# Kernel optimization log

Measured on AMD Instinct MI355X. Metric: run time of the kernel, lower is better.

The kernel has to match this reference:

```python
import jax, jax.numpy as jnp
import numpy as np


def setup_inputs() -> dict:
    key = jax.random.key(0)
    ks = jax.random.split(key, 7)
    B, L, D, H = 256, 1024, 768, 768
    x = jax.random.normal(ks[0], (B, L, D), dtype=jnp.float32)
    label_mask = jax.random.randint(ks[1], (B, L), 0, 2).astype(jnp.int32)
    global_prototype_tensor = jax.random.normal(ks[2], (L + 1, D), dtype=jnp.float32)
    W_h = jax.random.normal(ks[3], (H, D), dtype=jnp.float32) * 0.02
    b_h = jax.random.normal(ks[4], (H,), dtype=jnp.float32) * 0.02
    W_p = jax.random.normal(ks[5], (D, H), dtype=jnp.float32) * 0.02
    b_p = jax.random.normal(ks[6], (D,), dtype=jnp.float32) * 0.02
    return {"x": x, "label_mask": label_mask,
            "global_prototype_tensor": global_prototype_tensor,
            "W_h": W_h, "b_h": b_h, "W_p": W_p, "b_p": b_p}


def _mlp(v, W_h, b_h, W_p, b_p):
    # torch Linear: y = v @ W.T + b
    h = jax.nn.relu(jnp.einsum('ld,hd->lh', v, W_h) + b_h)
    return jnp.einsum('lh,dh->ld', h, W_p) + b_p


def reference(x, label_mask, global_prototype_tensor, W_h, b_h, W_p, b_p):
    # x: [B, L, D]; label_mask: [B, L] (1 if label i in example's label_list)
    m = label_mask.astype(x.dtype)                        # [B, L]
    pos_cnt = m.sum(0)                                    # [L]
    B = x.shape[0]
    anti_cnt = B - pos_cnt                                # [L]
    pos_sum = jnp.einsum('bl,bld->ld', m, x)              # masked segment-sum
    tot_sum = x.sum(0)                                    # [L, D]
    anti_sum = tot_sum - pos_sum

    pos_mean = pos_sum / jnp.maximum(pos_cnt, 1.0)[:, None]
    anti_mean = anti_sum / jnp.maximum(anti_cnt, 1.0)[:, None]

    avg_pos = 0.5 * pos_mean + 0.5 * global_prototype_tensor[:-1]   # [L, D]
    avg_anti = 0.5 * anti_mean + 0.5 * global_prototype_tensor[-1]  # [L, D]

    proto = _mlp(avg_pos, W_h, b_h, W_p, b_p)
    proto = jnp.where((pos_cnt > 0)[:, None], proto, 0.0)           # rows stay zero if no members

    anti_proto = _mlp(avg_anti, W_h, b_h, W_p, b_p)
    w = (anti_cnt > 0).astype(x.dtype)                              # [L]
    anti = jnp.einsum('l,ld->d', w, anti_proto) / jnp.maximum(w.sum(), 1.0)

    return jnp.concatenate([proto, anti[None, :]], axis=0)          # [L+1, D]
```

## Files before the change

### kernel.cpp

```cpp
#include <hip/hip_runtime.h>

#define L_DIM 1024
#define B_DIM 256
#define D_DIM 768
#define K_DIM 768
#define NT    (K_DIM / 32)

typedef short short8 __attribute__((ext_vector_type(8)));
typedef float floatx4 __attribute__((ext_vector_type(4)));

__device__ __forceinline__ ushort f2bf(float f) {
    union { float f; unsigned u; } v; v.f = f;
    unsigned r = v.u + 0x7FFF + ((v.u >> 16) & 1);
    return (ushort)(r >> 16);
}
__device__ __forceinline__ float bf2f(ushort h) {
    union { unsigned u; float f; } v; v.u = ((unsigned)h) << 16;
    return v.f;
}

__device__ __forceinline__ void gl16(const ushort* g, ushort* l) {
    __builtin_amdgcn_global_load_lds(
        (const __attribute__((address_space(1))) unsigned int*)g,
        (__attribute__((address_space(3))) unsigned int*)l, 16, 0, 0);
}

__global__ __launch_bounds__(768)
void reduce_build_v(const float* __restrict__ x,
                    const int* __restrict__ mask,
                    const float* __restrict__ gpt,
                    ushort* __restrict__ Vhi, ushort* __restrict__ Vlo,
                    float* __restrict__ pos_cnt)
{
    __shared__ int mS[256][4];

    const int l0  = blockIdx.x * 4;
    const int tid = threadIdx.x;

    if (tid < 256)
        *(int4*)&mS[tid][0] = *(const int4*)(mask + (size_t)tid * L_DIM + l0);
    __syncthreads();

    const int row = tid / 192;
    const int t   = tid % 192;
    const int d0  = t * 4;
    const int l   = l0 + row;

    const size_t bstride = (size_t)L_DIM * D_DIM;
    const float* xp = x + (size_t)l * D_DIM + d0;

    float4 pos = make_float4(0.f, 0.f, 0.f, 0.f);
    float4 tot = make_float4(0.f, 0.f, 0.f, 0.f);
    float cnt = 0.f;

    #pragma unroll 8
    for (int b = 0; b < B_DIM; ++b) {
        const float4 v = *(const float4*)(xp + (size_t)b * bstride);
        const float fm = (float)mS[b][row];
        tot.x += v.x; tot.y += v.y; tot.z += v.z; tot.w += v.w;
        pos.x = fmaf(fm, v.x, pos.x);
        pos.y = fmaf(fm, v.y, pos.y);
        pos.z = fmaf(fm, v.z, pos.z);
        pos.w = fmaf(fm, v.w, pos.w);
        cnt += fm;
    }

    const float inv_p = 0.5f / fmaxf(cnt, 1.0f);
    const float inv_a = 0.5f / fmaxf((float)B_DIM - cnt, 1.0f);

    const float4 g4  = *(const float4*)(gpt + (size_t)l * D_DIM + d0);
    const float4 gl4 = *(const float4*)(gpt + (size_t)L_DIM * D_DIM + d0);

    float vp[4], va[4];
    vp[0] = pos.x * inv_p + 0.5f * g4.x;
    vp[1] = pos.y * inv_p + 0.5f * g4.y;
    vp[2] = pos.z * inv_p + 0.5f * g4.z;
    vp[3] = pos.w * inv_p + 0.5f * g4.w;
    va[0] = (tot.x - pos.x) * inv_a + 0.5f * gl4.x;
    va[1] = (tot.y - pos.y) * inv_a + 0.5f * gl4.y;
    va[2] = (tot.z - pos.z) * inv_a + 0.5f * gl4.z;
    va[3] = (tot.w - pos.w) * inv_a + 0.5f * gl4.w;

    ushort4 ph, pl, ah, al;
    ph.x = f2bf(vp[0]); pl.x = f2bf(vp[0] - bf2f(ph.x));
    ph.y = f2bf(vp[1]); pl.y = f2bf(vp[1] - bf2f(ph.y));
    ph.z = f2bf(vp[2]); pl.z = f2bf(vp[2] - bf2f(ph.z));
    ph.w = f2bf(vp[3]); pl.w = f2bf(vp[3] - bf2f(ph.w));
    ah.x = f2bf(va[0]); al.x = f2bf(va[0] - bf2f(ah.x));
    ah.y = f2bf(va[1]); al.y = f2bf(va[1] - bf2f(ah.y));
    ah.z = f2bf(va[2]); al.z = f2bf(va[2] - bf2f(ah.z));
    ah.w = f2bf(va[3]); al.w = f2bf(va[3] - bf2f(ah.w));

    const size_t r0 = (size_t)l * D_DIM + d0;
    const size_t r1 = (size_t)(L_DIM + l) * D_DIM + d0;
    *(ushort4*)(Vhi + r0) = ph;  *(ushort4*)(Vlo + r0) = pl;
    *(ushort4*)(Vhi + r1) = ah;  *(ushort4*)(Vlo + r1) = al;

    if (t == 0) pos_cnt[l] = cnt;
}

__global__ __launch_bounds__(256)
void cast_w(const float* __restrict__ Wh, const float* __restrict__ Wp,
            ushort* __restrict__ WhHi, ushort* __restrict__ WhLo,
            ushort* __restrict__ WpHi, ushort* __restrict__ WpLo)
{
    const int n = 768 * 768;
    int i = (blockIdx.x * 256 + threadIdx.x) * 4;
    const float* src; ushort* dh; ushort* dl; int j;
    if (i < n) { src = Wh; dh = WhHi; dl = WhLo; j = i; }
    else       { src = Wp; dh = WpHi; dl = WpLo; j = i - n; }
    const float4 v = *(const float4*)(src + j);
    ushort4 hi, lo;
    hi.x = f2bf(v.x); lo.x = f2bf(v.x - bf2f(hi.x));
    hi.y = f2bf(v.y); lo.y = f2bf(v.y - bf2f(hi.y));
    hi.z = f2bf(v.z); lo.z = f2bf(v.z - bf2f(hi.z));
    hi.w = f2bf(v.w); lo.w = f2bf(v.w - bf2f(hi.w));
    *(ushort4*)(dh + j) = hi;
    *(ushort4*)(dl + j) = lo;
}

template<int MODE>
__global__ __launch_bounds__(256)
void gemm_split(const ushort* __restrict__ Ahi, const ushort* __restrict__ Alo,
                const ushort* __restrict__ Bhi, const ushort* __restrict__ Blo,
                const float* __restrict__ bias,
                ushort* __restrict__ OutHi, ushort* __restrict__ OutLo,
                float* __restrict__ OutF, float* __restrict__ Partial,
                const float* __restrict__ cnt)
{
    __shared__ ushort lds[2][4][64 * 32];
    __shared__ float  colsum[4][32];

    const int tid  = threadIdx.x;
    const int lane = tid & 63;
    const int wid  = tid >> 6;
    const int brow = blockIdx.y * 64;
    const int bcol = blockIdx.x * 64;
    const int wr   = (wid >> 1) * 32;
    const int wc   = (wid & 1) * 32;

    const int srow = tid >> 2;
    const int sk   = (tid & 3) * 8;

    const ushort* pAh = Ahi + (size_t)(brow + srow) * K_DIM + sk;
    const ushort* pAl = Alo + (size_t)(brow + srow) * K_DIM + sk;
    const ushort* pBh = Bhi + (size_t)(bcol + srow) * K_DIM + sk;
    const ushort* pBl = Blo + (size_t)(bcol + srow) * K_DIM + sk;

    const int ldst = tid * 8;
    const int fA0 = (wr +  0 + (lane & 15)) * 32 + (lane >> 4) * 8;
    const int fA1 = (wr + 16 + (lane & 15)) * 32 + (lane >> 4) * 8;
    const int fB0 = (wc +  0 + (lane & 15)) * 32 + (lane >> 4) * 8;
    const int fB1 = (wc + 16 + (lane & 15)) * 32 + (lane >> 4) * 8;

    floatx4 acc[2][2] = {};

    gl16(pAh, &lds[0][0][ldst]);
    gl16(pAl, &lds[0][1][ldst]);
    gl16(pBh, &lds[0][2][ldst]);
    gl16(pBl, &lds[0][3][ldst]);
    __syncthreads();

    for (int t = 0; t < NT; ++t) {
        const int cur = t & 1;
        if (t + 1 < NT) {
            const int ko = (t + 1) * 32;
            const int nxt = cur ^ 1;
            gl16(pAh + ko, &lds[nxt][0][ldst]);
            gl16(pAl + ko, &lds[nxt][1][ldst]);
            gl16(pBh + ko, &lds[nxt][2][ldst]);
            gl16(pBl + ko, &lds[nxt][3][ldst]);
        }
        short8 ah[2], al[2], bh[2], bl[2];
        ah[0] = *(short8*)&lds[cur][0][fA0];  ah[1] = *(short8*)&lds[cur][0][fA1];
        al[0] = *(short8*)&lds[cur][1][fA0];  al[1] = *(short8*)&lds[cur][1][fA1];
        bh[0] = *(short8*)&lds[cur][2][fB0];  bh[1] = *(short8*)&lds[cur][2][fB1];
        bl[0] = *(short8*)&lds[cur][3][fB0];  bl[1] = *(short8*)&lds[cur][3][fB1];
        #pragma unroll
        for (int mi = 0; mi < 2; ++mi)
            #pragma unroll
            for (int ni = 0; ni < 2; ++ni) {
                acc[mi][ni] = __builtin_amdgcn_mfma_f32_16x16x32_bf16(ah[mi], bh[ni], acc[mi][ni], 0, 0, 0);
                acc[mi][ni] = __builtin_amdgcn_mfma_f32_16x16x32_bf16(al[mi], bh[ni], acc[mi][ni], 0, 0, 0);
                acc[mi][ni] = __builtin_amdgcn_mfma_f32_16x16x32_bf16(ah[mi], bl[ni], acc[mi][ni], 0, 0, 0);
            }
        __syncthreads();
    }

    if (MODE == 0 || brow < L_DIM) {
        #pragma unroll
        for (int mi = 0; mi < 2; ++mi) {
            #pragma unroll
            for (int ni = 0; ni < 2; ++ni) {
                const int col   = bcol + wc + ni * 16 + (lane & 15);
                const int rbase = brow + wr + mi * 16 + ((lane >> 4) << 2);
                const float bv = bias[col];
                #pragma unroll
                for (int r = 0; r < 4; ++r) {
                    const float v = acc[mi][ni][r] + bv;
                    const int row = rbase + r;
                    if (MODE == 0) {
                        const float h = fmaxf(v, 0.f);
                        const ushort hh = f2bf(h);
                        OutHi[(size_t)row * D_DIM + col] = hh;
                        OutLo[(size_t)row * D_DIM + col] = f2bf(h - bf2f(hh));
                    } else {
                        OutF[(size_t)row * D_DIM + col] = (cnt[row] > 0.f) ? v : 0.f;
                    }
                }
            }
        }
    } else {
        float s[2] = {0.f, 0.f};
        #pragma unroll
        for (int mi = 0; mi < 2; ++mi) {
            const int rbase = brow + wr + mi * 16 + ((lane >> 4) << 2);
            #pragma unroll
            for (int r = 0; r < 4; ++r) {
                const float w = (cnt[rbase + r - L_DIM] < 255.5f) ? 1.0f : 0.0f;
                #pragma unroll
                for (int ni = 0; ni < 2; ++ni) {
                    const int col = bcol + wc + ni * 16 + (lane & 15);
                    s[ni] = fmaf(w, acc[mi][ni][r] + bias[col], s[ni]);
                }
            }
        }
        #pragma unroll
        for (int ni = 0; ni < 2; ++ni) {
            s[ni] += __shfl_down(s[ni], 32);
            s[ni] += __shfl_down(s[ni], 16);
            if (lane < 16) colsum[wid][ni * 16 + lane] = s[ni];
        }
        __syncthreads();
        if (tid < 64) {
            const float v = (tid < 32)
                ? colsum[0][tid] + colsum[2][tid]
                : colsum[1][tid - 32] + colsum[3][tid - 32];
            Partial[(size_t)(blockIdx.y - 16) * D_DIM + bcol + tid] = v;
        }
    }
}

__global__ __launch_bounds__(256)
void finalize_anti(const float* __restrict__ Partial,
                   const float* __restrict__ cnt,
                   float* __restrict__ out)
{
    const int d = blockIdx.x * 256 + threadIdx.x;
    float s = 0.f;
    #pragma unroll
    for (int p = 0; p < 16; ++p) s += Partial[(size_t)p * D_DIM + d];
    float wsum = 0.f;
    #pragma unroll 8
    for (int l = 0; l < L_DIM; ++l) wsum += (cnt[l] < 255.5f) ? 1.0f : 0.0f;
    out[(size_t)L_DIM * D_DIM + d] = s / fmaxf(wsum, 1.0f);
}

extern "C" void kernel_launch(void* const* d_in, const int* in_sizes, int n_in,
                              void* d_out, int out_size, void* d_ws, size_t ws_size,
                              hipStream_t stream) {
    const float* x    = (const float*)d_in[0];
    const int*   mask = (const int*)d_in[1];
    const float* gpt  = (const float*)d_in[2];
    const float* W_h  = (const float*)d_in[3];
    const float* b_h  = (const float*)d_in[4];
    const float* W_p  = (const float*)d_in[5];
    const float* b_p  = (const float*)d_in[6];
    float* out = (float*)d_out;

    char* p = (char*)d_ws;
    ushort* Vhi  = (ushort*)p; p += (size_t)2 * L_DIM * D_DIM * 2;
    ushort* Vlo  = (ushort*)p; p += (size_t)2 * L_DIM * D_DIM * 2;
    ushort* Hhi  = (ushort*)p; p += (size_t)2 * L_DIM * D_DIM * 2;
    ushort* Hlo  = (ushort*)p; p += (size_t)2 * L_DIM * D_DIM * 2;
    ushort* WhHi = (ushort*)p; p += (size_t)768 * 768 * 2;
    ushort* WhLo = (ushort*)p; p += (size_t)768 * 768 * 2;
    ushort* WpHi = (ushort*)p; p += (size_t)768 * 768 * 2;
    ushort* WpLo = (ushort*)p; p += (size_t)768 * 768 * 2;
    float*  Part = (float*)p;  p += (size_t)16 * D_DIM * 4;
    float*  cnt  = (float*)p;

    cast_w<<<(768 * 768 * 2 / 4) / 256, 256, 0, stream>>>(W_h, W_p, WhHi, WhLo, WpHi, WpLo);

    reduce_build_v<<<256, 768, 0, stream>>>(x, mask, gpt, Vhi, Vlo, cnt);

    dim3 ggrid(D_DIM / 64, 2 * L_DIM / 64);
    gemm_split<0><<<ggrid, 256, 0, stream>>>(Vhi, Vlo, WhHi, WhLo, b_h,
                                             Hhi, Hlo, nullptr, nullptr, nullptr);
    gemm_split<1><<<ggrid, 256, 0, stream>>>(Hhi, Hlo, WpHi, WpLo, b_p,
                                             nullptr, nullptr, out, Part, cnt);

    finalize_anti<<<3, 256, 0, stream>>>(Part, cnt, out);
}
```

Before: 206.5 us.

## Switch split-bf16 GEMMs to fp16 two-term split and fuse weight cast into reduction

The GEMMs move from a three-MFMA bf16 hi/lo split to fp16, where activations keep a hi/lo pair but weights use only a single fp16 term. That cuts MFMA count and LDS and global traffic for B by a third. The weight cast kernel is folded into the reduction kernel as extra blocks, which saves a launch. The x reduction now uses nontemporal loads with a deeper unroll, and LDS tiles get an XOR swizzle to reduce bank conflicts. Dropping the weight low term relies on fp16 mantissa precision being enough, and fp16 range limits add an accuracy risk.

```diff
diff --git a/kernel.cpp b/kernel.cpp
--- a/kernel.cpp
+++ b/kernel.cpp
@@ -5,18 +5,17 @@
 #define D_DIM 768
 #define K_DIM 768
 #define NT    (K_DIM / 32)
-
-typedef short short8 __attribute__((ext_vector_type(8)));
-typedef float floatx4 __attribute__((ext_vector_type(4)));
-
-__device__ __forceinline__ ushort f2bf(float f) {
-    union { float f; unsigned u; } v; v.f = f;
-    unsigned r = v.u + 0x7FFF + ((v.u >> 16) & 1);
-    return (ushort)(r >> 16);
-}
-__device__ __forceinline__ float bf2f(ushort h) {
-    union { unsigned u; float f; } v; v.u = ((unsigned)h) << 16;
-    return v.f;
+#define WN    (768 * 768)
+
+typedef _Float16 half8 __attribute__((ext_vector_type(8)));
+typedef float    floatx4 __attribute__((ext_vector_type(4)));
+
+__device__ __forceinline__ ushort f2h(float f) {
+    _Float16 h = (_Float16)f;
+    return __builtin_bit_cast(ushort, h);
+}
+__device__ __forceinline__ float h2f(ushort u) {
+    return (float)__builtin_bit_cast(_Float16, u);
 }
 
 __device__ __forceinline__ void gl16(const ushort* g, ushort* l) {
@@ -26,17 +25,29 @@
 }
 
 __global__ __launch_bounds__(768)
-void reduce_build_v(const float* __restrict__ x,
-                    const int* __restrict__ mask,
-                    const float* __restrict__ gpt,
-                    ushort* __restrict__ Vhi, ushort* __restrict__ Vlo,
-                    float* __restrict__ pos_cnt)
+void reduce_and_cast(const float* __restrict__ x,
+                     const int* __restrict__ mask,
+                     const float* __restrict__ gpt,
+                     const float* __restrict__ Wh, const float* __restrict__ Wp,
+                     ushort* __restrict__ Vhi, ushort* __restrict__ Vlo,
+                     ushort* __restrict__ WhH, ushort* __restrict__ WpH,
+                     float* __restrict__ pos_cnt)
 {
+    const int tid = threadIdx.x;
+
+    if (blockIdx.x >= 256) {
+        const int idx = ((blockIdx.x - 256) * 768 + tid) * 4;
+        const float4 v = (idx < WN) ? *(const float4*)(Wh + idx)
+                                    : *(const float4*)(Wp + (idx - WN));
+        ushort4 o;
+        o.x = f2h(v.x); o.y = f2h(v.y); o.z = f2h(v.z); o.w = f2h(v.w);
+        if (idx < WN) *(ushort4*)(WhH + idx) = o;
+        else          *(ushort4*)(WpH + (idx - WN)) = o;
+        return;
+    }
+
     __shared__ int mS[256][4];
-
-    const int l0  = blockIdx.x * 4;
-    const int tid = threadIdx.x;
-
+    const int l0 = blockIdx.x * 4;
     if (tid < 256)
         *(int4*)&mS[tid][0] = *(const int4*)(mask + (size_t)tid * L_DIM + l0);
     __syncthreads();
@@ -49,19 +60,19 @@
     const size_t bstride = (size_t)L_DIM * D_DIM;
     const float* xp = x + (size_t)l * D_DIM + d0;
 
-    float4 pos = make_float4(0.f, 0.f, 0.f, 0.f);
-    float4 tot = make_float4(0.f, 0.f, 0.f, 0.f);
+    floatx4 pos = {0.f, 0.f, 0.f, 0.f};
+    floatx4 tot = {0.f, 0.f, 0.f, 0.f};
     float cnt = 0.f;
 
-    #pragma unroll 8
+    #pragma unroll 16
     for (int b = 0; b < B_DIM; ++b) {
-        const float4 v = *(const float4*)(xp + (size_t)b * bstride);
+        const floatx4 v = __builtin_nontemporal_load((const floatx4*)(xp + (size_t)b * bstride));
         const float fm = (float)mS[b][row];
-        tot.x += v.x; tot.y += v.y; tot.z += v.z; tot.w += v.w;
-        pos.x = fmaf(fm, v.x, pos.x);
-        pos.y = fmaf(fm, v.y, pos.y);
-        pos.z = fmaf(fm, v.z, pos.z);
-        pos.w = fmaf(fm, v.w, pos.w);
+        tot += v;
+        pos[0] = fmaf(fm, v[0], pos[0]);
+        pos[1] = fmaf(fm, v[1], pos[1]);
+        pos[2] = fmaf(fm, v[2], pos[2]);
+        pos[3] = fmaf(fm, v[3], pos[3]);
         cnt += fm;
     }
 
@@ -72,24 +83,24 @@
     const float4 gl4 = *(const float4*)(gpt + (size_t)L_DIM * D_DIM + d0);
 
     float vp[4], va[4];
-    vp[0] = pos.x * inv_p + 0.5f * g4.x;
-    vp[1] = pos.y * inv_p + 0.5f * g4.y;
-    vp[2] = pos.z * inv_p + 0.5f * g4.z;
-    vp[3] = pos.w * inv_p + 0.5f * g4.w;
-    va[0] = (tot.x - pos.x) * inv_a + 0.5f * gl4.x;
-    va[1] = (tot.y - pos.y) * inv_a + 0.5f * gl4.y;
-    va[2] = (tot.z - pos.z) * inv_a + 0.5f * gl4.z;
-    va[3] = (tot.w - pos.w) * inv_a + 0.5f * gl4.w;
+    vp[0] = pos[0] * inv_p + 0.5f * g4.x;
+    vp[1] = pos[1] * inv_p + 0.5f * g4.y;
+    vp[2] = pos[2] * inv_p + 0.5f * g4.z;
+    vp[3] = pos[3] * inv_p + 0.5f * g4.w;
+    va[0] = (tot[0] - pos[0]) * inv_a + 0.5f * gl4.x;
+    va[1] = (tot[1] - pos[1]) * inv_a + 0.5f * gl4.y;
+    va[2] = (tot[2] - pos[2]) * inv_a + 0.5f * gl4.z;
+    va[3] = (tot[3] - pos[3]) * inv_a + 0.5f * gl4.w;
 
     ushort4 ph, pl, ah, al;
-    ph.x = f2bf(vp[0]); pl.x = f2bf(vp[0] - bf2f(ph.x));
-    ph.y = f2bf(vp[1]); pl.y = f2bf(vp[1] - bf2f(ph.y));
-    ph.z = f2bf(vp[2]); pl.z = f2bf(vp[2] - bf2f(ph.z));
-    ph.w = f2bf(vp[3]); pl.w = f2bf(vp[3] - bf2f(ph.w));
-    ah.x = f2bf(va[0]); al.x = f2bf(va[0] - bf2f(ah.x));
-    ah.y = f2bf(va[1]); al.y = f2bf(va[1] - bf2f(ah.y));
-    ah.z = f2bf(va[2]); al.z = f2bf(va[2] - bf2f(ah.z));
-    ah.w = f2bf(va[3]); al.w = f2bf(va[3] - bf2f(ah.w));
+    ph.x = f2h(vp[0]); pl.x = f2h(vp[0] - h2f(ph.x));
+    ph.y = f2h(vp[1]); pl.y = f2h(vp[1] - h2f(ph.y));
+    ph.z = f2h(vp[2]); pl.z = f2h(vp[2] - h2f(ph.z));
+    ph.w = f2h(vp[3]); pl.w = f2h(vp[3] - h2f(ph.w));
+    ah.x = f2h(va[0]); al.x = f2h(va[0] - h2f(ah.x));
+    ah.y = f2h(va[1]); al.y = f2h(va[1] - h2f(ah.y));
+    ah.z = f2h(va[2]); al.z = f2h(va[2] - h2f(ah.z));
+    ah.w = f2h(va[3]); al.w = f2h(va[3] - h2f(ah.w));
 
     const size_t r0 = (size_t)l * D_DIM + d0;
     const size_t r1 = (size_t)(L_DIM + l) * D_DIM + d0;
@@ -99,36 +110,15 @@
     if (t == 0) pos_cnt[l] = cnt;
 }
 
-__global__ __launch_bounds__(256)
-void cast_w(const float* __restrict__ Wh, const float* __restrict__ Wp,
-            ushort* __restrict__ WhHi, ushort* __restrict__ WhLo,
-            ushort* __restrict__ WpHi, ushort* __restrict__ WpLo)
-{
-    const int n = 768 * 768;
-    int i = (blockIdx.x * 256 + threadIdx.x) * 4;
-    const float* src; ushort* dh; ushort* dl; int j;
-    if (i < n) { src = Wh; dh = WhHi; dl = WhLo; j = i; }
-    else       { src = Wp; dh = WpHi; dl = WpLo; j = i - n; }
-    const float4 v = *(const float4*)(src + j);
-    ushort4 hi, lo;
-    hi.x = f2bf(v.x); lo.x = f2bf(v.x - bf2f(hi.x));
-    hi.y = f2bf(v.y); lo.y = f2bf(v.y - bf2f(hi.y));
-    hi.z = f2bf(v.z); lo.z = f2bf(v.z - bf2f(hi.z));
-    hi.w = f2bf(v.w); lo.w = f2bf(v.w - bf2f(hi.w));
-    *(ushort4*)(dh + j) = hi;
-    *(ushort4*)(dl + j) = lo;
-}
-
 template<int MODE>
 __global__ __launch_bounds__(256)
 void gemm_split(const ushort* __restrict__ Ahi, const ushort* __restrict__ Alo,
-                const ushort* __restrict__ Bhi, const ushort* __restrict__ Blo,
-                const float* __restrict__ bias,
+                const ushort* __restrict__ Bh, const float* __restrict__ bias,
                 ushort* __restrict__ OutHi, ushort* __restrict__ OutLo,
                 float* __restrict__ OutF, float* __restrict__ Partial,
                 const float* __restrict__ cnt)
 {
-    __shared__ ushort lds[2][4][64 * 32];
+    __shared__ ushort lds[2][3][64 * 32];
     __shared__ float  colsum[4][32];
 
     const int tid  = threadIdx.x;
@@ -140,25 +130,26 @@
     const int wc   = (wid & 1) * 32;
 
     const int srow = tid >> 2;
-    const int sk   = (tid & 3) * 8;
+    const int slot = tid & 3;
+    const int sk   = (slot ^ ((srow >> 1) & 3)) * 8;
 
     const ushort* pAh = Ahi + (size_t)(brow + srow) * K_DIM + sk;
     const ushort* pAl = Alo + (size_t)(brow + srow) * K_DIM + sk;
-    const ushort* pBh = Bhi + (size_t)(bcol + srow) * K_DIM + sk;
-    const ushort* pBl = Blo + (size_t)(bcol + srow) * K_DIM + sk;
+    const ushort* pBh = Bh  + (size_t)(bcol + srow) * K_DIM + sk;
 
     const int ldst = tid * 8;
-    const int fA0 = (wr +  0 + (lane & 15)) * 32 + (lane >> 4) * 8;
-    const int fA1 = (wr + 16 + (lane & 15)) * 32 + (lane >> 4) * 8;
-    const int fB0 = (wc +  0 + (lane & 15)) * 32 + (lane >> 4) * 8;
-    const int fB1 = (wc + 16 + (lane & 15)) * 32 + (lane >> 4) * 8;
+
+    const int q   = lane >> 4;
+    const int rA  = wr + (lane & 15);
+    const int rB  = wc + (lane & 15);
+    const int fA  = rA * 32 + ((q ^ ((rA >> 1) & 3)) << 3);
+    const int fB  = rB * 32 + ((q ^ ((rB >> 1) & 3)) << 3);
 
     floatx4 acc[2][2] = {};
 
     gl16(pAh, &lds[0][0][ldst]);
     gl16(pAl, &lds[0][1][ldst]);
     gl16(pBh, &lds[0][2][ldst]);
-    gl16(pBl, &lds[0][3][ldst]);
     __syncthreads();
 
     for (int t = 0; t < NT; ++t) {
@@ -169,21 +160,23 @@
             gl16(pAh + ko, &lds[nxt][0][ldst]);
             gl16(pAl + ko, &lds[nxt][1][ldst]);
             gl16(pBh + ko, &lds[nxt][2][ldst]);
-            gl16(pBl + ko, &lds[nxt][3][ldst]);
-        }
-        short8 ah[2], al[2], bh[2], bl[2];
-        ah[0] = *(short8*)&lds[cur][0][fA0];  ah[1] = *(short8*)&lds[cur][0][fA1];
-        al[0] = *(short8*)&lds[cur][1][fA0];  al[1] = *(short8*)&lds[cur][1][fA1];
-        bh[0] = *(short8*)&lds[cur][2][fB0];  bh[1] = *(short8*)&lds[cur][2][fB1];
-        bl[0] = *(short8*)&lds[cur][3][fB0];  bl[1] = *(short8*)&lds[cur][3][fB1];
-        #pragma unroll
-        for (int mi = 0; mi < 2; ++mi)
-            #pragma unroll
-            for (int ni = 0; ni < 2; ++ni) {
-                acc[mi][ni] = __builtin_amdgcn_mfma_f32_16x16x32_bf16(ah[mi], bh[ni], acc[mi][ni], 0, 0, 0);
-                acc[mi][ni] = __builtin_amdgcn_mfma_f32_16x16x32_bf16(al[mi], bh[ni], acc[mi][ni], 0, 0, 0);
-                acc[mi][ni] = __builtin_amdgcn_mfma_f32_16x16x32_bf16(ah[mi], bl[ni], acc[mi][ni], 0, 0, 0);
-            }
+        }
+        half8 ah0 = *(half8*)&lds[cur][0][fA];
+        half8 ah1 = *(half8*)&lds[cur][0][fA + 512];
+        half8 al0 = *(half8*)&lds[cur][1][fA];
+        half8 al1 = *(half8*)&lds[cur][1][fA + 512];
+        half8 bh0 = *(half8*)&lds[cur][2][fB];
+        half8 bh1 = *(half8*)&lds[cur][2][fB + 512];
+
+        acc[0][0] = __builtin_amdgcn_mfma_f32_16x16x32_f16(ah0, bh0, acc[0][0], 0, 0, 0);
+        acc[0][1] = __builtin_amdgcn_mfma_f32_16x16x32_f16(ah0, bh1, acc[0][1], 0, 0, 0);
+        acc[1][0] = __builtin_amdgcn_mfma_f32_16x16x32_f16(ah1, bh0, acc[1][0], 0, 0, 0);
+        acc[1][1] = __builtin_amdgcn_mfma_f32_16x16x32_f16(ah1, bh1, acc[1][1], 0, 0, 0);
+        acc[0][0] = __builtin_amdgcn_mfma_f32_16x16x32_f16(al0, bh0, acc[0][0], 0, 0, 0);
+        acc[0][1] = __builtin_amdgcn_mfma_f32_16x16x32_f16(al0, bh1, acc[0][1], 0, 0, 0);
+        acc[1][0] = __builtin_amdgcn_mfma_f32_16x16x32_f16(al1, bh0, acc[1][0], 0, 0, 0);
+        acc[1][1] = __builtin_amdgcn_mfma_f32_16x16x32_f16(al1, bh1, acc[1][1], 0, 0, 0);
+
         __syncthreads();
     }
 
@@ -201,9 +194,9 @@
                     const int row = rbase + r;
                     if (MODE == 0) {
                         const float h = fmaxf(v, 0.f);
-                        const ushort hh = f2bf(h);
+                        const ushort hh = f2h(h);
                         OutHi[(size_t)row * D_DIM + col] = hh;
-                        OutLo[(size_t)row * D_DIM + col] = f2bf(h - bf2f(hh));
+                        OutLo[(size_t)row * D_DIM + col] = f2h(h - h2f(hh));
                     } else {
                         OutF[(size_t)row * D_DIM + col] = (cnt[row] > 0.f) ? v : 0.f;
                     }
@@ -273,21 +266,18 @@
     ushort* Vlo  = (ushort*)p; p += (size_t)2 * L_DIM * D_DIM * 2;
     ushort* Hhi  = (ushort*)p; p += (size_t)2 * L_DIM * D_DIM * 2;
     ushort* Hlo  = (ushort*)p; p += (size_t)2 * L_DIM * D_DIM * 2;
-    ushort* WhHi = (ushort*)p; p += (size_t)768 * 768 * 2;
-    ushort* WhLo = (ushort*)p; p += (size_t)768 * 768 * 2;
-    ushort* WpHi = (ushort*)p; p += (size_t)768 * 768 * 2;
-    ushort* WpLo = (ushort*)p; p += (size_t)768 * 768 * 2;
+    ushort* WhH  = (ushort*)p; p += (size_t)WN * 2;
+    ushort* WpH  = (ushort*)p; p += (size_t)WN * 2;
     float*  Part = (float*)p;  p += (size_t)16 * D_DIM * 4;
     float*  cnt  = (float*)p;
 
-    cast_w<<<(768 * 768 * 2 / 4) / 256, 256, 0, stream>>>(W_h, W_p, WhHi, WhLo, WpHi, WpLo);
-
-    reduce_build_v<<<256, 768, 0, stream>>>(x, mask, gpt, Vhi, Vlo, cnt);
+    reduce_and_cast<<<640, 768, 0, stream>>>(x, mask, gpt, W_h, W_p,
+                                             Vhi, Vlo, WhH, WpH, cnt);
 
     dim3 ggrid(D_DIM / 64, 2 * L_DIM / 64);
-    gemm_split<0><<<ggrid, 256, 0, stream>>>(Vhi, Vlo, WhHi, WhLo, b_h,
+    gemm_split<0><<<ggrid, 256, 0, stream>>>(Vhi, Vlo, WhH, b_h,
                                              Hhi, Hlo, nullptr, nullptr, nullptr);
-    gemm_split<1><<<ggrid, 256, 0, stream>>>(Hhi, Hlo, WpHi, WpLo, b_p,
+    gemm_split<1><<<ggrid, 256, 0, stream>>>(Hhi, Hlo, WpH, b_p,
                                              nullptr, nullptr, out, Part, cnt);
 
     finalize_anti<<<3, 256, 0, stream>>>(Part, cnt, out);
```

Result: faster. 187.0 us (-9.4%).
